# Kernel optimization log

Measured on AMD Instinct MI355X. Metric: run time of the kernel, lower is better.

The kernel has to match this reference:

```python
import jax, jax.numpy as jnp
import numpy as np

MIN_POS = 1e-6
EPS = 1e-20
B, S, F_IN, E, H = 2, 1024, 768, 768, 12
DH = E // H   # nnmf in_features per head (64)
FH = E // H   # nnmf out_features per head (hidden_features=embed_dim default)
N_NNMF_ITERS = 3
N_ALPHA_ITERS = 3


def l1norm(x, axis=-1):
    # F.normalize(x, p=1, dim=axis, eps=1e-20) for non-negative x
    return x / jnp.maximum(jnp.sum(jnp.abs(x), axis=axis, keepdims=True), EPS)


def setup_inputs() -> dict:
    key = jax.random.key(0)
    k = jax.random.split(key, 6)
    return {
        "x": jax.random.normal(k[0], (B, S, F_IN), jnp.float32),
        "embed_w": jax.random.normal(k[1], (E, F_IN), jnp.float32) * 0.02,
        "embed_b": jnp.zeros((E,), jnp.float32),
        "nnmf_w": jax.random.uniform(k[2], (FH, DH), jnp.float32),  # non-negative NMF dictionary
        "out_w": jax.random.normal(k[3], (F_IN, E), jnp.float32) * 0.02,
        "out_b": jnp.zeros((F_IN,), jnp.float32),
    }


def reference(x, embed_w, embed_b, nnmf_w, out_w, out_b):
    # normalize NMF weight rows (p=1 over in_features), as nnmf_layer.normalize_weights
    W = nnmf_w / jnp.maximum(jnp.sum(nnmf_w, axis=1, keepdims=True), EPS)  # [FH, DH]

    # embed + clamp positive, split heads
    xe = jnp.clip(x @ embed_w.T + embed_b, MIN_POS)            # [B,S,E]
    xe = xe.reshape(B, S, H, DH)                                # [B,S,H,DH]

    # NNMFDense: prepared_input = l1-normalized input (normalize_input_dim=-1)
    inp = l1norm(xe)                                            # [B,S,H,DH]
    h = l1norm(jnp.ones((B, S, H, FH), x.dtype))                # init hidden
    rec = inp
    for _ in range(N_NNMF_ITERS):
        rec = l1norm(jnp.clip(h @ W, MIN_POS))                  # reconstruction [B,S,H,DH]
        h = l1norm(jnp.clip(h * ((inp / rec) @ W.T), MIN_POS))  # multiplicative update

    # normalize_h (p=1, dim=-1)
    h = l1norm(h)                                               # [B,S,H,FH] -> 'bohf'

    # alpha dynamics fixed point
    alpha = jnp.ones((B, H, S, S), x.dtype)                     # 'bhoi'
    h_rec_input = rec * inp                                     # [B,S,H,DH]
    for _ in range(N_ALPHA_ITERS):
        h_mixed = jnp.einsum('bohf,bhoi->bihf', h, alpha)       # [B,S,H,FH]
        arec_inv = 1.0 / (h_mixed @ W + EPS)                    # _reconstruct -> [B,S,H,DH]
        alpha = alpha * jnp.einsum('bohf,bihf->bhoi', h_rec_input, arec_inv)

    out = jnp.einsum('bohf,bhoi->bihf', h, alpha)               # [B,S,H,FH]
    out = out.reshape(B, S, E)                                  # flatten heads
    return out @ out_w.T + out_b                                # out_project
```

## Files before the change

### kernel.cpp

```cpp
#include <hip/hip_runtime.h>

#define B_  2
#define S_  1024
#define FIN 768
#define E_  768
#define H_  12
#define DH  64

typedef unsigned int uint;
typedef unsigned short ushort;
typedef __attribute__((ext_vector_type(8))) short short8;
typedef __attribute__((ext_vector_type(4))) float floatx4;

__device__ __forceinline__ ushort f2bf(float f) {
    uint u = __float_as_uint(f);
    return (ushort)((u + 0x7fffu + ((u >> 16) & 1u)) >> 16);
}

__device__ __forceinline__ uint4 pack8(const ushort* p) {
    uint4 r;
    r.x = (uint)p[0] | ((uint)p[1] << 16);
    r.y = (uint)p[2] | ((uint)p[3] << 16);
    r.z = (uint)p[4] | ((uint)p[5] << 16);
    r.w = (uint)p[6] | ((uint)p[7] << 16);
    return r;
}

__device__ __forceinline__ void split8v(float4 a, float4 b, short8& hi, short8& lo) {
    float v[8] = {a.x, a.y, a.z, a.w, b.x, b.y, b.z, b.w};
    ushort h[8], l[8];
#pragma unroll
    for (int j = 0; j < 8; ++j) {
        h[j] = f2bf(v[j]);
        l[j] = f2bf(v[j] - __uint_as_float(((uint)h[j]) << 16));
    }
    uint4 H = pack8(h), L = pack8(l);
    hi = *(short8*)&H;
    lo = *(short8*)&L;
}

__global__ __launch_bounds__(256) void k_conv(const float* __restrict__ xs,
                                              const float* __restrict__ ew,
                                              const float* __restrict__ nw,
                                              ushort* __restrict__ xsH,
                                              ushort* __restrict__ xsL,
                                              ushort* __restrict__ ewH,
                                              ushort* __restrict__ ewL,
                                              float* __restrict__ Wn,
                                              float* __restrict__ r1inv,
                                              ushort* __restrict__ Wfrag) {
    __shared__ float Wl[64 * 65];
    const int tid = threadIdx.x, bid = blockIdx.x;

    if (bid < 768) {
        const size_t i = ((size_t)bid * 256 + tid) * 8;
        short8 hi, lo;
        split8v(*(const float4*)(xs + i), *(const float4*)(xs + i + 4), hi, lo);
        *(short8*)(xsH + i) = hi;
        *(short8*)(xsL + i) = lo;
        return;
    }
    if (bid < 1056) {
        const size_t i = ((size_t)(bid - 768) * 256 + tid) * 8;
        short8 hi, lo;
        split8v(*(const float4*)(ew + i), *(const float4*)(ew + i + 4), hi, lo);
        *(short8*)(ewH + i) = hi;
        *(short8*)(ewL + i) = lo;
        return;
    }

    const int f = tid >> 2, q = tid & 3;
    float v[16];
    float s = 0.f;
#pragma unroll
    for (int i = 0; i < 16; ++i) { v[i] = nw[f * 64 + q * 16 + i]; s += v[i]; }
    s += __shfl_xor(s, 1, 64);
    s += __shfl_xor(s, 2, 64);
    const float inv = 1.f / fmaxf(s, 1e-20f);
    float w[16];
#pragma unroll
    for (int i = 0; i < 16; ++i) {
        w[i] = v[i] * inv;
        Wn[f * 64 + q * 16 + i] = w[i];
        Wl[f * 65 + q * 16 + i] = w[i];
    }
    __syncthreads();
    if (tid < 64) {
        float cs = 0.f;
        for (int ff = 0; ff < 64; ++ff) cs += Wl[ff * 65 + tid];
        float t = fmaxf(cs * (1.f / 64.f), 1e-6f);
        float S = t;
#pragma unroll
        for (int m = 1; m < 64; m <<= 1) S += __shfl_xor(S, m, 64);
        S = fmaxf(S, 1e-20f);
        r1inv[tid] = S / t;
    }
    {
        short8 h0, l0, h1, l1;
        split8v(make_float4(w[0], w[1], w[2], w[3]),
                make_float4(w[4], w[5], w[6], w[7]), h0, l0);
        split8v(make_float4(w[8], w[9], w[10], w[11]),
                make_float4(w[12], w[13], w[14], w[15]), h1, l1);
        ushort* WwH = Wfrag + 2 * 4096;
        ushort* WwL = Wfrag + 3 * 4096;
        *(short8*)(WwH + f * 64 + q * 16) = h0;
        *(short8*)(WwH + f * 64 + q * 16 + 8) = h1;
        *(short8*)(WwL + f * 64 + q * 16) = l0;
        *(short8*)(WwL + f * 64 + q * 16 + 8) = l1;
    }
    {
        float t[16];
#pragma unroll
        for (int i = 0; i < 16; ++i) t[i] = Wl[(q * 16 + i) * 65 + f];
        short8 h0, l0, h1, l1;
        split8v(make_float4(t[0], t[1], t[2], t[3]),
                make_float4(t[4], t[5], t[6], t[7]), h0, l0);
        split8v(make_float4(t[8], t[9], t[10], t[11]),
                make_float4(t[12], t[13], t[14], t[15]), h1, l1);
        ushort* WtH = Wfrag;
        ushort* WtL = Wfrag + 4096;
        *(short8*)(WtH + f * 64 + q * 16) = h0;
        *(short8*)(WtH + f * 64 + q * 16 + 8) = h1;
        *(short8*)(WtL + f * 64 + q * 16) = l0;
        *(short8*)(WtL + f * 64 + q * 16 + 8) = l1;
    }
}

__global__ __launch_bounds__(256) void k_embed(const ushort* __restrict__ xsH,
                                               const ushort* __restrict__ xsL,
                                               const ushort* __restrict__ ewH,
                                               const ushort* __restrict__ ewL,
                                               const float* __restrict__ eb,
                                               float* __restrict__ inp) {
    __shared__ ushort AsH[2][64 * 72], AsL[2][64 * 72];
    __shared__ ushort BsH[2][64 * 72], BsL[2][64 * 72];
    const int tid = threadIdx.x;
    const int bid = blockIdx.x;

    const int head = bid % 12;
    const int tok0 = (bid / 12) * 64;

    const int wv = tid >> 6, lane = tid & 63;
    const int mbase = wv * 16;
    const int lm = lane & 15, lq = lane >> 4;

    floatx4 accA[4], accB[4];
#pragma unroll
    for (int nt = 0; nt < 4; ++nt) { accA[nt] = (floatx4)0.f; accB[nt] = (floatx4)0.f; }

    const int srow = tid >> 2, skq = (tid & 3) * 16;
    const int off = srow * 72 + skq;
    const ushort* xh = xsH + (size_t)(tok0 + srow) * FIN + skq;
    const ushort* xl = xsL + (size_t)(tok0 + srow) * FIN + skq;
    const ushort* wh = ewH + (size_t)(head * 64 + srow) * FIN + skq;
    const ushort* wl = ewL + (size_t)(head * 64 + srow) * FIN + skq;

    short8 pa[4], pb[4];
    pa[0] = *(const short8*)(xh);  pa[1] = *(const short8*)(xh + 8);
    pa[2] = *(const short8*)(xl);  pa[3] = *(const short8*)(xl + 8);
    pb[0] = *(const short8*)(wh);  pb[1] = *(const short8*)(wh + 8);
    pb[2] = *(const short8*)(wl);  pb[3] = *(const short8*)(wl + 8);
    *(short8*)&AsH[0][off]     = pa[0];
    *(short8*)&AsH[0][off + 8] = pa[1];
    *(short8*)&AsL[0][off]     = pa[2];
    *(short8*)&AsL[0][off + 8] = pa[3];
    *(short8*)&BsH[0][off]     = pb[0];
    *(short8*)&BsH[0][off + 8] = pb[1];
    *(short8*)&BsL[0][off]     = pb[2];
    *(short8*)&BsL[0][off + 8] = pb[3];
    pa[0] = *(const short8*)(xh + 64);  pa[1] = *(const short8*)(xh + 72);
    pa[2] = *(const short8*)(xl + 64);  pa[3] = *(const short8*)(xl + 72);
    pb[0] = *(const short8*)(wh + 64);  pb[1] = *(const short8*)(wh + 72);
    pb[2] = *(const short8*)(wl + 64);  pb[3] = *(const short8*)(wl + 72);
    __syncthreads();

#pragma unroll 2
    for (int kb = 0; kb < 12; ++kb) {
        const int cur = kb & 1;
#pragma unroll
        for (int ch = 0; ch < 2; ++ch) {
            const int ko = ch * 32 + lq * 8;
            short8 ah = *(const short8*)&AsH[cur][(mbase + lm) * 72 + ko];
            short8 al = *(const short8*)&AsL[cur][(mbase + lm) * 72 + ko];
#pragma unroll
            for (int nt = 0; nt < 4; ++nt) {
                short8 bh = *(const short8*)&BsH[cur][(nt * 16 + lm) * 72 + ko];
                short8 bl = *(const short8*)&BsL[cur][(nt * 16 + lm) * 72 + ko];
                accA[nt] = __builtin_amdgcn_mfma_f32_16x16x32_bf16(ah, bh, accA[nt], 0, 0, 0);
                accB[nt] = __builtin_amdgcn_mfma_f32_16x16x32_bf16(al, bh, accB[nt], 0, 0, 0);
                accB[nt] = __builtin_amdgcn_mfma_f32_16x16x32_bf16(ah, bl, accB[nt], 0, 0, 0);
            }
        }
        if (kb + 1 < 12) {
            *(short8*)&AsH[cur ^ 1][off]     = pa[0];
            *(short8*)&AsH[cur ^ 1][off + 8] = pa[1];
            *(short8*)&AsL[cur ^ 1][off]     = pa[2];
            *(short8*)&AsL[cur ^ 1][off + 8] = pa[3];
            *(short8*)&BsH[cur ^ 1][off]     = pb[0];
            *(short8*)&BsH[cur ^ 1][off + 8] = pb[1];
            *(short8*)&BsL[cur ^ 1][off]     = pb[2];
            *(short8*)&BsL[cur ^ 1][off + 8] = pb[3];
        }
        if (kb + 2 < 12) {
            const int ko = (kb + 2) * 64;
            pa[0] = *(const short8*)(xh + ko);  pa[1] = *(const short8*)(xh + ko + 8);
            pa[2] = *(const short8*)(xl + ko);  pa[3] = *(const short8*)(xl + ko + 8);
            pb[0] = *(const short8*)(wh + ko);  pb[1] = *(const short8*)(wh + ko + 8);
            pb[2] = *(const short8*)(wl + ko);  pb[3] = *(const short8*)(wl + ko + 8);
        }
        __syncthreads();
    }

    float bb[4];
#pragma unroll
    for (int nt = 0; nt < 4; ++nt) bb[nt] = eb[head * 64 + nt * 16 + lm];
    const size_t obase = ((size_t)((tok0 >> 10) * 12 + head) * 1024 + (tok0 & 1023));
#pragma unroll
    for (int r = 0; r < 4; ++r) {
        float e[4];
        float p = 0.f;
#pragma unroll
        for (int nt = 0; nt < 4; ++nt) {
            e[nt] = fmaxf((accA[nt][r] + accB[nt][r]) + bb[nt], 1e-6f);
            p += e[nt];
        }
        p += __shfl_xor(p, 1, 64);
        p += __shfl_xor(p, 2, 64);
        p += __shfl_xor(p, 4, 64);
        p += __shfl_xor(p, 8, 64);
        const float inv = 1.f / fmaxf(p, 1e-20f);
        const int m = mbase + lq * 4 + r;
        float* op = inp + (obase + m) * 64;
#pragma unroll
        for (int nt = 0; nt < 4; ++nt)
            op[nt * 16 + lm] = e[nt] * inv;
    }
}

__device__ __forceinline__ void mfma_matvec(const float srcC[4][4], float* T,
                                            int lm, int lq,
                                            const ushort* WH, const ushort* WL,
                                            floatx4 out[4]) {
    __builtin_amdgcn_wave_barrier();
#pragma unroll
    for (int nt = 0; nt < 4; ++nt)
#pragma unroll
        for (int r = 0; r < 4; ++r)
            T[(lq * 4 + r) * 68 + nt * 16 + lm] = srcC[nt][r];
    __builtin_amdgcn_wave_barrier();
    float4 a00 = *(const float4*)&T[lm * 68 + lq * 8];
    float4 a01 = *(const float4*)&T[lm * 68 + lq * 8 + 4];
    float4 a10 = *(const float4*)&T[lm * 68 + 32 + lq * 8];
    float4 a11 = *(const float4*)&T[lm * 68 + 32 + lq * 8 + 4];
    __builtin_amdgcn_wave_barrier();
    short8 A0h, A0l, A1h, A1l;
    split8v(a00, a01, A0h, A0l);
    split8v(a10, a11, A1h, A1l);
#pragma unroll
    for (int nt = 0; nt < 4; ++nt) {
        const int row = (nt * 16 + lm) * 72;
        short8 b0h = *(const short8*)&WH[row + lq * 8];
        short8 b0l = *(const short8*)&WL[row + lq * 8];
        short8 b1h = *(const short8*)&WH[row + 32 + lq * 8];
        short8 b1l = *(const short8*)&WL[row + 32 + lq * 8];
        floatx4 acc0 = (floatx4)0.f, acc1 = (floatx4)0.f;
        acc0 = __builtin_amdgcn_mfma_f32_16x16x32_bf16(A0h, b0h, acc0, 0, 0, 0);
        acc0 = __builtin_amdgcn_mfma_f32_16x16x32_bf16(A0l, b0h, acc0, 0, 0, 0);
        acc0 = __builtin_amdgcn_mfma_f32_16x16x32_bf16(A0h, b0l, acc0, 0, 0, 0);
        acc1 = __builtin_amdgcn_mfma_f32_16x16x32_bf16(A1h, b1h, acc1, 0, 0, 0);
        acc1 = __builtin_amdgcn_mfma_f32_16x16x32_bf16(A1l, b1h, acc1, 0, 0, 0);
        acc1 = __builtin_amdgcn_mfma_f32_16x16x32_bf16(A1h, b1l, acc1, 0, 0, 0);
        out[nt] = acc0 + acc1;
    }
}

__global__ __launch_bounds__(256) void k_nnmf(const float* __restrict__ inp,
                                              const ushort* __restrict__ Wfrag,
                                              const float* __restrict__ r1inv,
                                              float* __restrict__ hout,
                                              float* __restrict__ hriout,
                                              float* __restrict__ mp0) {
    __shared__ ushort WtH[64 * 72], WtL[64 * 72];
    __shared__ ushort WwH[64 * 72], WwL[64 * 72];
    __shared__ float Tb[4][16 * 68];
    __shared__ float pbuf[256];
    const int tid = threadIdx.x, wv = tid >> 6, lane = tid & 63;
    const int lm = lane & 15, lq = lane >> 4;
    float* T = Tb[wv];
    const int rowbase = blockIdx.x * 64 + wv * 16;

    {
        const int row = tid >> 2, kq = (tid & 3) * 16;
        const int g = row * 64 + kq, l = row * 72 + kq;
        *(short8*)&WtH[l]     = *(const short8*)(Wfrag + g);
        *(short8*)&WtH[l + 8] = *(const short8*)(Wfrag + g + 8);
        *(short8*)&WtL[l]     = *(const short8*)(Wfrag + 4096 + g);
        *(short8*)&WtL[l + 8] = *(const short8*)(Wfrag + 4096 + g + 8);
        *(short8*)&WwH[l]     = *(const short8*)(Wfrag + 8192 + g);
        *(short8*)&WwH[l + 8] = *(const short8*)(Wfrag + 8192 + g + 8);
        *(short8*)&WwL[l]     = *(const short8*)(Wfrag + 12288 + g);
        *(short8*)&WwL[l + 8] = *(const short8*)(Wfrag + 12288 + g + 8);
    }

    float inpC[4][4];
#pragma unroll
    for (int nt = 0; nt < 4; ++nt)
#pragma unroll
        for (int r = 0; r < 4; ++r)
            inpC[nt][r] = inp[(size_t)(rowbase + lq * 4 + r) * 64 + nt * 16 + lm];
    float r1c[4];
#pragma unroll
    for (int nt = 0; nt < 4; ++nt) r1c[nt] = r1inv[nt * 16 + lm];
    __syncthreads();

    float hC[4][4], recC[4][4];
    {
        float qC[4][4];
#pragma unroll
        for (int nt = 0; nt < 4; ++nt)
#pragma unroll
            for (int r = 0; r < 4; ++r) qC[nt][r] = inpC[nt][r] * r1c[nt];
        floatx4 u[4];
        mfma_matvec(qC, T, lm, lq, WwH, WwL, u);
#pragma unroll
        for (int nt = 0; nt < 4; ++nt)
#pragma unroll
            for (int r = 0; r < 4; ++r)
                hC[nt][r] = fmaxf(u[nt][r] * (1.f / 64.f), 1e-6f);
#pragma unroll
        for (int r = 0; r < 4; ++r) {
            float s = (hC[0][r] + hC[1][r]) + (hC[2][r] + hC[3][r]);
            s += __shfl_xor(s, 1, 64); s += __shfl_xor(s, 2, 64);
            s += __shfl_xor(s, 4, 64); s += __shfl_xor(s, 8, 64);
            const float inv = __builtin_amdgcn_rcpf(fmaxf(s, 1e-20f));
#pragma unroll
            for (int nt = 0; nt < 4; ++nt) hC[nt][r] *= inv;
        }
    }
#pragma unroll 1
    for (int it = 0; it < 2; ++it) {
        floatx4 t[4];
        mfma_matvec(hC, T, lm, lq, WtH, WtL, t);
        float tC[4][4], qC[4][4];
#pragma unroll
        for (int nt = 0; nt < 4; ++nt)
#pragma unroll
            for (int r = 0; r < 4; ++r) tC[nt][r] = fmaxf(t[nt][r], 1e-6f);
#pragma unroll
        for (int r = 0; r < 4; ++r) {
            float s = (tC[0][r] + tC[1][r]) + (tC[2][r] + tC[3][r]);
            s += __shfl_xor(s, 1, 64); s += __shfl_xor(s, 2, 64);
            s += __shfl_xor(s, 4, 64); s += __shfl_xor(s, 8, 64);
            s = fmaxf(s, 1e-20f);
            const float invS = __builtin_amdgcn_rcpf(s);
#pragma unroll
            for (int nt = 0; nt < 4; ++nt) {
                recC[nt][r] = tC[nt][r] * invS;
                qC[nt][r] = inpC[nt][r] * s * __builtin_amdgcn_rcpf(tC[nt][r]);
            }
        }
        floatx4 u[4];
        mfma_matvec(qC, T, lm, lq, WwH, WwL, u);
#pragma unroll
        for (int nt = 0; nt < 4; ++nt)
#pragma unroll
            for (int r = 0; r < 4; ++r)
                hC[nt][r] = fmaxf(hC[nt][r] * u[nt][r], 1e-6f);
#pragma unroll
        for (int r = 0; r < 4; ++r) {
            float s = (hC[0][r] + hC[1][r]) + (hC[2][r] + hC[3][r]);
            s += __shfl_xor(s, 1, 64); s += __shfl_xor(s, 2, 64);
            s += __shfl_xor(s, 4, 64); s += __shfl_xor(s, 8, 64);
            const float inv = __builtin_amdgcn_rcpf(fmaxf(s, 1e-20f));
#pragma unroll
            for (int nt = 0; nt < 4; ++nt) hC[nt][r] *= inv;
        }
    }
#pragma unroll
    for (int r = 0; r < 4; ++r) {
        float s = (hC[0][r] + hC[1][r]) + (hC[2][r] + hC[3][r]);
        s += __shfl_xor(s, 1, 64); s += __shfl_xor(s, 2, 64);
        s += __shfl_xor(s, 4, 64); s += __shfl_xor(s, 8, 64);
        const float inv = __builtin_amdgcn_rcpf(fmaxf(s, 1e-20f));
#pragma unroll
        for (int nt = 0; nt < 4; ++nt) hC[nt][r] *= inv;
    }

#pragma unroll
    for (int nt = 0; nt < 4; ++nt)
#pragma unroll
        for (int r = 0; r < 4; ++r) {
            const size_t o = (size_t)(rowbase + lq * 4 + r) * 64 + nt * 16 + lm;
            hout[o] = hC[nt][r];
            hriout[o] = recC[nt][r] * inpC[nt][r];
        }

    float hs[4];
#pragma unroll
    for (int nt = 0; nt < 4; ++nt) {
        float s = (hC[nt][0] + hC[nt][1]) + (hC[nt][2] + hC[nt][3]);
        s += __shfl_xor(s, 16, 64);
        s += __shfl_xor(s, 32, 64);
        hs[nt] = s;
    }
    pbuf[wv * 64 + lq * 16 + lm] = hs[lq];
    __syncthreads();
    if (tid < 64) {
        float tot = (pbuf[tid] + pbuf[64 + tid]) + (pbuf[128 + tid] + pbuf[192 + tid]);
        mp0[(size_t)blockIdx.x * 64 + tid] = tot;
    }
}

__global__ __launch_bounds__(256) void k_alpha_step(const float* __restrict__ hin,
                                                    const float* __restrict__ hri,
                                                    const float* __restrict__ Wn,
                                                    const float* __restrict__ mp_in,
                                                    float* __restrict__ mp_out,
                                                    float* __restrict__ c,
                                                    int it) {
    __shared__ float mred[4][64];
    __shared__ float mv[64];
    __shared__ float vv[64];
    __shared__ float cl[64];
    const int tid = threadIdx.x;
    const int bh = blockIdx.x >> 4;
    const int chunk = blockIdx.x & 15;
    const size_t rowbase = (size_t)bh * 1024 + chunk * 64;

    {
        int f = tid & 63, p = tid >> 6;
        float s = 0.f;
#pragma unroll
        for (int pp = 0; pp < 4; ++pp)
            s += mp_in[((size_t)bh * 16 + p * 4 + pp) * 64 + f];
        mred[p][f] = s;
    }
    __syncthreads();
    if (tid < 64)
        mv[tid] = (mred[0][tid] + mred[1][tid]) + (mred[2][tid] + mred[3][tid]);
    __syncthreads();
    {
        int d = tid & 63, qq = tid >> 6;
        float r = 0.f;
#pragma unroll
        for (int ff = 0; ff < 16; ++ff)
            r = fmaf(mv[qq * 16 + ff], Wn[(size_t)(qq * 16 + ff) * 64 + d], r);
        mred[qq][d] = r;
    }
    __syncthreads();
    if (tid < 64)
        vv[tid] = 1.f / (((mred[0][tid] + mred[1][tid]) + (mred[2][tid] + mred[3][tid])) + 1e-20f);
    __syncthreads();
    {
        int o = tid >> 2, dq = tid & 3;
        const float* rp = hri + (rowbase + o) * 64 + dq * 16;
        float dot = 0.f;
#pragma unroll
        for (int t4 = 0; t4 < 16; t4 += 4) {
            float4 r4 = *(const float4*)(rp + t4);
            dot = fmaf(r4.x, vv[dq * 16 + t4 + 0], dot);
            dot = fmaf(r4.y, vv[dq * 16 + t4 + 1], dot);
            dot = fmaf(r4.z, vv[dq * 16 + t4 + 2], dot);
            dot = fmaf(r4.w, vv[dq * 16 + t4 + 3], dot);
        }
        dot += __shfl_xor(dot, 1, 64);
        dot += __shfl_xor(dot, 2, 64);
        float cn = dot;
        if (it >= 2) cn *= c[rowbase + o];
        if (dq == 0) { c[rowbase + o] = cn; cl[o] = cn; }
    }
    __syncthreads();
    {
        const int f4 = (tid & 15) * 4, ogr = tid >> 4;
        float4 a = make_float4(0.f, 0.f, 0.f, 0.f);
#pragma unroll
        for (int oi = 0; oi < 4; ++oi) {
            int o = ogr * 4 + oi;
            float4 h4 = *(const float4*)(hin + (rowbase + o) * 64 + f4);
            float cv = cl[o];
            a.x = fmaf(h4.x, cv, a.x); a.y = fmaf(h4.y, cv, a.y);
            a.z = fmaf(h4.z, cv, a.z); a.w = fmaf(h4.w, cv, a.w);
        }
        a.x += __shfl_xor(a.x, 16, 64); a.y += __shfl_xor(a.y, 16, 64);
        a.z += __shfl_xor(a.z, 16, 64); a.w += __shfl_xor(a.w, 16, 64);
        a.x += __shfl_xor(a.x, 32, 64); a.y += __shfl_xor(a.y, 32, 64);
        a.z += __shfl_xor(a.z, 32, 64); a.w += __shfl_xor(a.w, 32, 64);
        const int w = tid >> 6;
        if ((tid & 63) < 16) *(float4*)&mred[w][(tid & 15) * 4] = a;
    }
    __syncthreads();
    if (tid < 64) {
        float s = (mred[0][tid] + mred[1][tid]) + (mred[2][tid] + mred[3][tid]);
        mp_out[((size_t)bh * 16 + chunk) * 64 + tid] = s;
    }
}

__global__ __launch_bounds__(256) void k_projbcast(const float* __restrict__ mp3,
                                                   const float* __restrict__ ow,
                                                   const float* __restrict__ ob,
                                                   float* __restrict__ out) {
    __shared__ float Ml[768];
    __shared__ float ps[4][64];
    __shared__ float yseg[64];
    const int tid = threadIdx.x;
    const int b = blockIdx.x / 192;
    const int rem = blockIdx.x - b * 192;
    const int jt = rem >> 4, rg = rem & 15;
    for (int i = tid; i < 768; i += 256) {
        const int hh = i >> 6, f = i & 63;
        const float* src = mp3 + ((size_t)(b * 12 + hh) * 16) * 64 + f;
        float s = 0.f;
#pragma unroll
        for (int cc = 0; cc < 16; ++cc) s += src[cc * 64];
        Ml[i] = s;
    }
    __syncthreads();
    const int jj = tid & 63, part = tid >> 6;
    const int j = jt * 64 + jj;
    const float* row = ow + (size_t)j * 768 + part * 192;
    float acc = 0.f;
    for (int t = 0; t < 192; t += 4) {
        float4 w4 = *(const float4*)(row + t);
        acc = fmaf(w4.x, Ml[part * 192 + t + 0], acc);
        acc = fmaf(w4.y, Ml[part * 192 + t + 1], acc);
        acc = fmaf(w4.z, Ml[part * 192 + t + 2], acc);
        acc = fmaf(w4.w, Ml[part * 192 + t + 3], acc);
    }
    ps[part][jj] = acc;
    __syncthreads();
    if (tid < 64)
        yseg[tid] = ps[0][tid] + ps[1][tid] + ps[2][tid] + ps[3][tid] + ob[jt * 64 + tid];
    __syncthreads();
    const int r0 = tid >> 2, c4 = (tid & 3) * 16;
    float4 v4[4];
#pragma unroll
    for (int q = 0; q < 4; ++q) v4[q] = *(const float4*)&yseg[c4 + q * 4];
    float* dst = out + ((size_t)(b * 1024 + rg * 64 + r0)) * 768 + jt * 64 + c4;
#pragma unroll
    for (int q = 0; q < 4; ++q) *(float4*)(dst + q * 4) = v4[q];
}

extern "C" void kernel_launch(void* const* d_in, const int* in_sizes, int n_in,
                              void* d_out, int out_size, void* d_ws, size_t ws_size,
                              hipStream_t stream) {
    const float* xs = (const float*)d_in[0];
    const float* ew = (const float*)d_in[1];
    const float* eb = (const float*)d_in[2];
    const float* nw = (const float*)d_in[3];
    const float* ow = (const float*)d_in[4];
    const float* ob = (const float*)d_in[5];
    float* out = (float*)d_out;

    float* ws    = (float*)d_ws;
    float* inp   = ws;
    float* h     = ws + 1572864;
    float* hri   = ws + 3145728;
    float* Wn    = ws + 4718592;
    float* r1inv = ws + 4722688;
    float* mp0   = ws + 4722944;
    float* mp1   = ws + 4747520;
    float* mp2   = ws + 4772096;
    float* c     = ws + 4796672;
    ushort* xsH  = (ushort*)(ws + 4821248);
    ushort* xsL  = (ushort*)(ws + 5607680);
    ushort* ewH  = (ushort*)(ws + 6394112);
    ushort* ewL  = (ushort*)(ws + 6689024);
    ushort* Wfrag= (ushort*)(ws + 6983936);

    k_conv<<<1057, 256, 0, stream>>>(xs, ew, nw, xsH, xsL, ewH, ewL, Wn, r1inv, Wfrag);
    k_embed<<<384, 256, 0, stream>>>(xsH, xsL, ewH, ewL, eb, inp);
    k_nnmf<<<384, 256, 0, stream>>>(inp, Wfrag, r1inv, h, hri, mp0);
    k_alpha_step<<<384, 256, 0, stream>>>(h, hri, Wn, mp0, mp1, c, 1);
    k_alpha_step<<<384, 256, 0, stream>>>(h, hri, Wn, mp1, mp2, c, 2);
    k_alpha_step<<<384, 256, 0, stream>>>(h, hri, Wn, mp2, mp1, c, 3);
    k_projbcast<<<384, 256, 0, stream>>>(mp1, ow, ob, out);
}
```

Measured before the change: 131.5 us.

## Fuse embed GEMM into NNMF kernel, keeping normalized input in registers

Merges the embedding GEMM kernel and the NNMF iteration kernel into one launch. The normalized embedding output now stays in registers and goes straight into the NNMF updates, so the inp buffer is no longer written to and re-read from global memory. Shared memory is one 72KB buffer reused between the GEMM staging tiles and the NNMF weight and transpose buffers. Larger shared memory use per block may reduce occupancy.

```diff
diff --git a/kernel.cpp b/kernel.cpp
--- a/kernel.cpp
+++ b/kernel.cpp
@@ -123,117 +123,6 @@
         *(short8*)(WtH + f * 64 + q * 16 + 8) = h1;
         *(short8*)(WtL + f * 64 + q * 16) = l0;
         *(short8*)(WtL + f * 64 + q * 16 + 8) = l1;
-    }
-}
-
-__global__ __launch_bounds__(256) void k_embed(const ushort* __restrict__ xsH,
-                                               const ushort* __restrict__ xsL,
-                                               const ushort* __restrict__ ewH,
-                                               const ushort* __restrict__ ewL,
-                                               const float* __restrict__ eb,
-                                               float* __restrict__ inp) {
-    __shared__ ushort AsH[2][64 * 72], AsL[2][64 * 72];
-    __shared__ ushort BsH[2][64 * 72], BsL[2][64 * 72];
-    const int tid = threadIdx.x;
-    const int bid = blockIdx.x;
-
-    const int head = bid % 12;
-    const int tok0 = (bid / 12) * 64;
-
-    const int wv = tid >> 6, lane = tid & 63;
-    const int mbase = wv * 16;
-    const int lm = lane & 15, lq = lane >> 4;
-
-    floatx4 accA[4], accB[4];
-#pragma unroll
-    for (int nt = 0; nt < 4; ++nt) { accA[nt] = (floatx4)0.f; accB[nt] = (floatx4)0.f; }
-
-    const int srow = tid >> 2, skq = (tid & 3) * 16;
-    const int off = srow * 72 + skq;
-    const ushort* xh = xsH + (size_t)(tok0 + srow) * FIN + skq;
-    const ushort* xl = xsL + (size_t)(tok0 + srow) * FIN + skq;
-    const ushort* wh = ewH + (size_t)(head * 64 + srow) * FIN + skq;
-    const ushort* wl = ewL + (size_t)(head * 64 + srow) * FIN + skq;
-
-    short8 pa[4], pb[4];
-    pa[0] = *(const short8*)(xh);  pa[1] = *(const short8*)(xh + 8);
-    pa[2] = *(const short8*)(xl);  pa[3] = *(const short8*)(xl + 8);
-    pb[0] = *(const short8*)(wh);  pb[1] = *(const short8*)(wh + 8);
-    pb[2] = *(const short8*)(wl);  pb[3] = *(const short8*)(wl + 8);
-    *(short8*)&AsH[0][off]     = pa[0];
-    *(short8*)&AsH[0][off + 8] = pa[1];
-    *(short8*)&AsL[0][off]     = pa[2];
-    *(short8*)&AsL[0][off + 8] = pa[3];
-    *(short8*)&BsH[0][off]     = pb[0];
-    *(short8*)&BsH[0][off + 8] = pb[1];
-    *(short8*)&BsL[0][off]     = pb[2];
-    *(short8*)&BsL[0][off + 8] = pb[3];
-    pa[0] = *(const short8*)(xh + 64);  pa[1] = *(const short8*)(xh + 72);
-    pa[2] = *(const short8*)(xl + 64);  pa[3] = *(const short8*)(xl + 72);
-    pb[0] = *(const short8*)(wh + 64);  pb[1] = *(const short8*)(wh + 72);
-    pb[2] = *(const short8*)(wl + 64);  pb[3] = *(const short8*)(wl + 72);
-    __syncthreads();
-
-#pragma unroll 2
-    for (int kb = 0; kb < 12; ++kb) {
-        const int cur = kb & 1;
-#pragma unroll
-        for (int ch = 0; ch < 2; ++ch) {
-            const int ko = ch * 32 + lq * 8;
-            short8 ah = *(const short8*)&AsH[cur][(mbase + lm) * 72 + ko];
-            short8 al = *(const short8*)&AsL[cur][(mbase + lm) * 72 + ko];
-#pragma unroll
-            for (int nt = 0; nt < 4; ++nt) {
-                short8 bh = *(const short8*)&BsH[cur][(nt * 16 + lm) * 72 + ko];
-                short8 bl = *(const short8*)&BsL[cur][(nt * 16 + lm) * 72 + ko];
-                accA[nt] = __builtin_amdgcn_mfma_f32_16x16x32_bf16(ah, bh, accA[nt], 0, 0, 0);
-                accB[nt] = __builtin_amdgcn_mfma_f32_16x16x32_bf16(al, bh, accB[nt], 0, 0, 0);
-                accB[nt] = __builtin_amdgcn_mfma_f32_16x16x32_bf16(ah, bl, accB[nt], 0, 0, 0);
-            }
-        }
-        if (kb + 1 < 12) {
-            *(short8*)&AsH[cur ^ 1][off]     = pa[0];
-            *(short8*)&AsH[cur ^ 1][off + 8] = pa[1];
-            *(short8*)&AsL[cur ^ 1][off]     = pa[2];
-            *(short8*)&AsL[cur ^ 1][off + 8] = pa[3];
-            *(short8*)&BsH[cur ^ 1][off]     = pb[0];
-            *(short8*)&BsH[cur ^ 1][off + 8] = pb[1];
-            *(short8*)&BsL[cur ^ 1][off]     = pb[2];
-            *(short8*)&BsL[cur ^ 1][off + 8] = pb[3];
-        }
-        if (kb + 2 < 12) {
-            const int ko = (kb + 2) * 64;
-            pa[0] = *(const short8*)(xh + ko);  pa[1] = *(const short8*)(xh + ko + 8);
-            pa[2] = *(const short8*)(xl + ko);  pa[3] = *(const short8*)(xl + ko + 8);
-            pb[0] = *(const short8*)(wh + ko);  pb[1] = *(const short8*)(wh + ko + 8);
-            pb[2] = *(const short8*)(wl + ko);  pb[3] = *(const short8*)(wl + ko + 8);
-        }
-        __syncthreads();
-    }
-
-    float bb[4];
-#pragma unroll
-    for (int nt = 0; nt < 4; ++nt) bb[nt] = eb[head * 64 + nt * 16 + lm];
-    const size_t obase = ((size_t)((tok0 >> 10) * 12 + head) * 1024 + (tok0 & 1023));
-#pragma unroll
-    for (int r = 0; r < 4; ++r) {
-        float e[4];
-        float p = 0.f;
-#pragma unroll
-        for (int nt = 0; nt < 4; ++nt) {
-            e[nt] = fmaxf((accA[nt][r] + accB[nt][r]) + bb[nt], 1e-6f);
-            p += e[nt];
-        }
-        p += __shfl_xor(p, 1, 64);
-        p += __shfl_xor(p, 2, 64);
-        p += __shfl_xor(p, 4, 64);
-        p += __shfl_xor(p, 8, 64);
-        const float inv = 1.f / fmaxf(p, 1e-20f);
-        const int m = mbase + lq * 4 + r;
-        float* op = inp + (obase + m) * 64;
-#pragma unroll
-        for (int nt = 0; nt < 4; ++nt)
-            op[nt * 16 + lm] = e[nt] * inv;
     }
 }
 
@@ -274,44 +163,161 @@
     }
 }
 
-__global__ __launch_bounds__(256) void k_nnmf(const float* __restrict__ inp,
-                                              const ushort* __restrict__ Wfrag,
-                                              const float* __restrict__ r1inv,
-                                              float* __restrict__ hout,
-                                              float* __restrict__ hriout,
-                                              float* __restrict__ mp0) {
-    __shared__ ushort WtH[64 * 72], WtL[64 * 72];
-    __shared__ ushort WwH[64 * 72], WwL[64 * 72];
-    __shared__ float Tb[4][16 * 68];
-    __shared__ float pbuf[256];
-    const int tid = threadIdx.x, wv = tid >> 6, lane = tid & 63;
+__global__ __launch_bounds__(256) void k_embed_nnmf(const ushort* __restrict__ xsH,
+                                                    const ushort* __restrict__ xsL,
+                                                    const ushort* __restrict__ ewH,
+                                                    const ushort* __restrict__ ewL,
+                                                    const float* __restrict__ eb,
+                                                    const ushort* __restrict__ Wfrag,
+                                                    const float* __restrict__ r1inv,
+                                                    float* __restrict__ hout,
+                                                    float* __restrict__ hriout,
+                                                    float* __restrict__ mp0) {
+    __shared__ __align__(16) unsigned char smem[73728];
+    ushort* const sm = (ushort*)smem;
+    const int tid = threadIdx.x;
+    const int bid = blockIdx.x;
+
+    const int head = bid % 12;
+    const int tok0 = (bid / 12) * 64;
+
+    const int wv = tid >> 6, lane = tid & 63;
+    const int mbase = wv * 16;
     const int lm = lane & 15, lq = lane >> 4;
-    float* T = Tb[wv];
-    const int rowbase = blockIdx.x * 64 + wv * 16;
-
-    {
-        const int row = tid >> 2, kq = (tid & 3) * 16;
-        const int g = row * 64 + kq, l = row * 72 + kq;
-        *(short8*)&WtH[l]     = *(const short8*)(Wfrag + g);
-        *(short8*)&WtH[l + 8] = *(const short8*)(Wfrag + g + 8);
-        *(short8*)&WtL[l]     = *(const short8*)(Wfrag + 4096 + g);
-        *(short8*)&WtL[l + 8] = *(const short8*)(Wfrag + 4096 + g + 8);
-        *(short8*)&WwH[l]     = *(const short8*)(Wfrag + 8192 + g);
-        *(short8*)&WwH[l + 8] = *(const short8*)(Wfrag + 8192 + g + 8);
-        *(short8*)&WwL[l]     = *(const short8*)(Wfrag + 12288 + g);
-        *(short8*)&WwL[l + 8] = *(const short8*)(Wfrag + 12288 + g + 8);
-    }
+
+    floatx4 accA[4], accB[4];
+#pragma unroll
+    for (int nt = 0; nt < 4; ++nt) { accA[nt] = (floatx4)0.f; accB[nt] = (floatx4)0.f; }
+
+    const int srow = tid >> 2, skq = (tid & 3) * 16;
+    const int off = srow * 72 + skq;
+    const ushort* xh = xsH + (size_t)(tok0 + srow) * FIN + skq;
+    const ushort* xl = xsL + (size_t)(tok0 + srow) * FIN + skq;
+    const ushort* wh = ewH + (size_t)(head * 64 + srow) * FIN + skq;
+    const ushort* wl = ewL + (size_t)(head * 64 + srow) * FIN + skq;
+
+    short8 pa[4], pb[4];
+    pa[0] = *(const short8*)(xh);  pa[1] = *(const short8*)(xh + 8);
+    pa[2] = *(const short8*)(xl);  pa[3] = *(const short8*)(xl + 8);
+    pb[0] = *(const short8*)(wh);  pb[1] = *(const short8*)(wh + 8);
+    pb[2] = *(const short8*)(wl);  pb[3] = *(const short8*)(wl + 8);
+    {
+        ushort* b0 = sm;
+        *(short8*)&b0[off]            = pa[0];
+        *(short8*)&b0[off + 8]        = pa[1];
+        *(short8*)&b0[4608 + off]     = pa[2];
+        *(short8*)&b0[4608 + off + 8] = pa[3];
+        *(short8*)&b0[9216 + off]     = pb[0];
+        *(short8*)&b0[9216 + off + 8] = pb[1];
+        *(short8*)&b0[13824 + off]    = pb[2];
+        *(short8*)&b0[13824 + off + 8]= pb[3];
+    }
+    pa[0] = *(const short8*)(xh + 64);  pa[1] = *(const short8*)(xh + 72);
+    pa[2] = *(const short8*)(xl + 64);  pa[3] = *(const short8*)(xl + 72);
+    pb[0] = *(const short8*)(wh + 64);  pb[1] = *(const short8*)(wh + 72);
+    pb[2] = *(const short8*)(wl + 64);  pb[3] = *(const short8*)(wl + 72);
+    __syncthreads();
+
+#pragma unroll 2
+    for (int kb = 0; kb < 12; ++kb) {
+        const int cur = kb & 1;
+        const ushort* cb = sm + cur * 18432;
+#pragma unroll
+        for (int ch = 0; ch < 2; ++ch) {
+            const int ko = ch * 32 + lq * 8;
+            short8 ah = *(const short8*)&cb[(mbase + lm) * 72 + ko];
+            short8 al = *(const short8*)&cb[4608 + (mbase + lm) * 72 + ko];
+#pragma unroll
+            for (int nt = 0; nt < 4; ++nt) {
+                short8 bh = *(const short8*)&cb[9216 + (nt * 16 + lm) * 72 + ko];
+                short8 bl = *(const short8*)&cb[13824 + (nt * 16 + lm) * 72 + ko];
+                accA[nt] = __builtin_amdgcn_mfma_f32_16x16x32_bf16(ah, bh, accA[nt], 0, 0, 0);
+                accB[nt] = __builtin_amdgcn_mfma_f32_16x16x32_bf16(al, bh, accB[nt], 0, 0, 0);
+                accB[nt] = __builtin_amdgcn_mfma_f32_16x16x32_bf16(ah, bl, accB[nt], 0, 0, 0);
+            }
+        }
+        if (kb + 1 < 12) {
+            ushort* sb = sm + (cur ^ 1) * 18432;
+            *(short8*)&sb[off]            = pa[0];
+            *(short8*)&sb[off + 8]        = pa[1];
+            *(short8*)&sb[4608 + off]     = pa[2];
+            *(short8*)&sb[4608 + off + 8] = pa[3];
+            *(short8*)&sb[9216 + off]     = pb[0];
+            *(short8*)&sb[9216 + off + 8] = pb[1];
+            *(short8*)&sb[13824 + off]    = pb[2];
+            *(short8*)&sb[13824 + off + 8]= pb[3];
+        }
+        if (kb + 2 < 12) {
+            const int ko = (kb + 2) * 64;
+            pa[0] = *(const short8*)(xh + ko);  pa[1] = *(const short8*)(xh + ko + 8);
+            pa[2] = *(const short8*)(xl + ko);  pa[3] = *(const short8*)(xl + ko + 8);
+            pb[0] = *(const short8*)(wh + ko);  pb[1] = *(const short8*)(wh + ko + 8);
+            pb[2] = *(const short8*)(wl + ko);  pb[3] = *(const short8*)(wl + ko + 8);
+        }
+        __syncthreads();
+    }
+
+    const int wrow = tid >> 2, wkq = (tid & 3) * 16;
+    const int wg = wrow * 64 + wkq;
+    short8 wt0 = *(const short8*)(Wfrag + wg);
+    short8 wt1 = *(const short8*)(Wfrag + wg + 8);
+    short8 wt2 = *(const short8*)(Wfrag + 4096 + wg);
+    short8 wt3 = *(const short8*)(Wfrag + 4096 + wg + 8);
+    short8 ww0 = *(const short8*)(Wfrag + 8192 + wg);
+    short8 ww1 = *(const short8*)(Wfrag + 8192 + wg + 8);
+    short8 ww2 = *(const short8*)(Wfrag + 12288 + wg);
+    short8 ww3 = *(const short8*)(Wfrag + 12288 + wg + 8);
+    float r1c[4];
+#pragma unroll
+    for (int nt = 0; nt < 4; ++nt) r1c[nt] = r1inv[nt * 16 + lm];
 
     float inpC[4][4];
-#pragma unroll
-    for (int nt = 0; nt < 4; ++nt)
-#pragma unroll
-        for (int r = 0; r < 4; ++r)
-            inpC[nt][r] = inp[(size_t)(rowbase + lq * 4 + r) * 64 + nt * 16 + lm];
-    float r1c[4];
-#pragma unroll
-    for (int nt = 0; nt < 4; ++nt) r1c[nt] = r1inv[nt * 16 + lm];
-    __syncthreads();
+    {
+        float bb[4];
+#pragma unroll
+        for (int nt = 0; nt < 4; ++nt) bb[nt] = eb[head * 64 + nt * 16 + lm];
+#pragma unroll
+        for (int r = 0; r < 4; ++r) {
+            float e[4];
+            float p = 0.f;
+#pragma unroll
+            for (int nt = 0; nt < 4; ++nt) {
+                e[nt] = fmaxf((accA[nt][r] + accB[nt][r]) + bb[nt], 1e-6f);
+                p += e[nt];
+            }
+            p += __shfl_xor(p, 1, 64);
+            p += __shfl_xor(p, 2, 64);
+            p += __shfl_xor(p, 4, 64);
+            p += __shfl_xor(p, 8, 64);
+            const float inv = 1.f / fmaxf(p, 1e-20f);
+#pragma unroll
+            for (int nt = 0; nt < 4; ++nt) inpC[nt][r] = e[nt] * inv;
+        }
+    }
+
+    __syncthreads();
+    ushort* WtH = sm;
+    ushort* WtL = sm + 4608;
+    ushort* WwH = sm + 9216;
+    ushort* WwL = sm + 13824;
+    float*  Tb  = (float*)(smem + 36864);
+    float*  pbuf= (float*)(smem + 54272);
+    float*  T   = Tb + wv * (16 * 68);
+    {
+        const int l = wrow * 72 + wkq;
+        *(short8*)&WtH[l]     = wt0;
+        *(short8*)&WtH[l + 8] = wt1;
+        *(short8*)&WtL[l]     = wt2;
+        *(short8*)&WtL[l + 8] = wt3;
+        *(short8*)&WwH[l]     = ww0;
+        *(short8*)&WwH[l + 8] = ww1;
+        *(short8*)&WwL[l]     = ww2;
+        *(short8*)&WwL[l + 8] = ww3;
+    }
+    __syncthreads();
+
+    const size_t obase = ((size_t)((tok0 >> 10) * 12 + head) * 1024 + (tok0 & 1023));
+    const size_t rowbase = obase + wv * 16;
 
     float hC[4][4], recC[4][4];
     {
@@ -390,7 +396,7 @@
     for (int nt = 0; nt < 4; ++nt)
 #pragma unroll
         for (int r = 0; r < 4; ++r) {
-            const size_t o = (size_t)(rowbase + lq * 4 + r) * 64 + nt * 16 + lm;
+            const size_t o = (rowbase + lq * 4 + r) * 64 + nt * 16 + lm;
             hout[o] = hC[nt][r];
             hriout[o] = recC[nt][r] * inpC[nt][r];
         }
@@ -407,7 +413,7 @@
     __syncthreads();
     if (tid < 64) {
         float tot = (pbuf[tid] + pbuf[64 + tid]) + (pbuf[128 + tid] + pbuf[192 + tid]);
-        mp0[(size_t)blockIdx.x * 64 + tid] = tot;
+        mp0[(obase >> 6) * 64 + tid] = tot;
     }
 }
 
@@ -552,7 +558,6 @@
     float* out = (float*)d_out;
 
     float* ws    = (float*)d_ws;
-    float* inp   = ws;
     float* h     = ws + 1572864;
     float* hri   = ws + 3145728;
     float* Wn    = ws + 4718592;
@@ -568,8 +573,7 @@
     ushort* Wfrag= (ushort*)(ws + 6983936);
 
     k_conv<<<1057, 256, 0, stream>>>(xs, ew, nw, xsH, xsL, ewH, ewL, Wn, r1inv, Wfrag);
-    k_embed<<<384, 256, 0, stream>>>(xsH, xsL, ewH, ewL, eb, inp);
-    k_nnmf<<<384, 256, 0, stream>>>(inp, Wfrag, r1inv, h, hri, mp0);
+    k_embed_nnmf<<<384, 256, 0, stream>>>(xsH, xsL, ewH, ewL, eb, Wfrag, r1inv, h, hri, mp0);
     k_alpha_step<<<384, 256, 0, stream>>>(h, hri, Wn, mp0, mp1, c, 1);
     k_alpha_step<<<384, 256, 0, stream>>>(h, hri, Wn, mp1, mp2, c, 2);
     k_alpha_step<<<384, 256, 0, stream>>>(h, hri, Wn, mp2, mp1, c, 3);
```

New measurement: 128.3 us, median of 2. -2.5%, faster.
